# Kernel optimization log

Measured on AMD Instinct MI355X. Metric: run time of the kernel, lower is better.

The kernel has to match this reference:

```python
import jax, jax.numpy as jnp
import numpy as np

B = 128  # number of graphs/molecules in batch


def setup_inputs() -> dict:
    key = jax.random.key(0)
    ks = jax.random.split(key, 6)
    T, C, D = 131072, 512, 512  # total nodes, feature_dim, out_dim
    hidden_states = jax.random.normal(ks[0], (T, C), dtype=jnp.float32)
    data_batch = jnp.sort(jax.random.randint(ks[1], (T,), 0, B, dtype=jnp.int32))
    lim1 = 1.0 / np.sqrt(C)
    lim2 = 1.0 / np.sqrt(D)
    return {
        "hidden_states": hidden_states,
        "data_batch": data_batch,
        "max_nodes": 1280,
        "ln_gamma": jnp.ones((C,), jnp.float32),
        "ln_beta": jnp.zeros((C,), jnp.float32),
        "W1": jax.random.uniform(ks[2], (D, C), jnp.float32, -lim1, lim1),
        "b1": jax.random.uniform(ks[3], (D,), jnp.float32, -lim1, lim1),
        "W2": jax.random.uniform(ks[4], (D, D), jnp.float32, -lim2, lim2),
        "b2": jax.random.uniform(ks[5], (D,), jnp.float32, -lim2, lim2),
    }


def reference(hidden_states, data_batch, max_nodes, ln_gamma, ln_beta, W1, b1, W2, b2):
    T, C = hidden_states.shape
    # ragged -> dense scatter: position of each node within its batch group
    counts = jnp.bincount(data_batch, length=B)               # [B]
    offsets = jnp.cumsum(counts) - counts                      # exclusive cumsum [B]
    pos = jnp.arange(T, dtype=jnp.int32) - offsets[data_batch]  # [T]
    result = jnp.zeros((B, max_nodes, C), hidden_states.dtype).at[data_batch, pos].set(hidden_states)
    # mask: a padded row is all-zero
    mask = jnp.any(result != 0, axis=-1)[..., None].astype(result.dtype)  # [B, N, 1]
    # LayerNorm (eps=1e-5, torch default)
    mu = jnp.mean(result, axis=-1, keepdims=True)
    var = jnp.mean((result - mu) ** 2, axis=-1, keepdims=True)
    logits = (result - mu) * jax.lax.rsqrt(var + 1e-5) * ln_gamma + ln_beta
    cap_embes = logits @ W1.T + b1                              # [B, N, D]
    features_in = cap_embes @ W2.T + b2                         # [B, N, D]
    features_in = jnp.where(mask == 0, -10000.0, features_in)
    attn = jax.nn.softmax(features_in, axis=1)                  # softmax over nodes
    attn = jnp.where(mask == 0, 0.0, attn)
    return jnp.sum(attn * cap_embes, axis=1)                    # [B, D]
```

## Files before the change

### kernel.cpp

```cpp
#include <hip/hip_runtime.h>
#include <hip/hip_bf16.h>


typedef short short8 __attribute__((ext_vector_type(8)));
typedef short short4v __attribute__((ext_vector_type(4)));
typedef float f32x4 __attribute__((ext_vector_type(4)));

__device__ inline short f2bf(float f) {
    unsigned u = __float_as_uint(f);
    u += 0x7fffu + ((u >> 16) & 1u);
    return (short)(u >> 16);
}

__device__ inline size_t packed_off(int n, int k) {
    const int t = n >> 4, l16 = n & 15;
    const int k0 = k >> 5, quad = (k >> 3) & 3, j = k & 7;
    return ((size_t)((t * 16 + k0) * 64 + quad * 16 + l16)) * 8 + j;
}

#define PREP_GRID 229

__global__ __launch_bounds__(512)
void esa_prep_all(const float* __restrict__ W1, const float* __restrict__ W2,
                  const float* __restrict__ b1, const float* __restrict__ b2,
                  const int* __restrict__ db, int T, int B,
                  short* __restrict__ W1p, short* __restrict__ W12p,
                  float* __restrict__ b12, int4* __restrict__ entries, int maxent,
                  float* __restrict__ numden) {
    __shared__ int off[513];
    __shared__ int nch[512];
    __shared__ int scan[513];
    const int bid = blockIdx.x;
    const int tid = threadIdx.x;

    if (bid < 64) {
        const int ti = bid >> 3, tj = bid & 7;
        const int wave = tid >> 6;
        const int lane = tid & 63;
        const int quad = lane >> 4;
        const int l16 = lane & 15;
        const int mhalf = wave >> 2;
        const int kq = wave & 3;
        const int kcol = tj * 64 + kq * 16 + l16;

        f32x4 acc[2];
        acc[0] = (f32x4)0.0f; acc[1] = (f32x4)0.0f;
        for (int j0 = 0; j0 < 512; j0 += 32) {
            short8 bfr;
#pragma unroll
            for (int jj = 0; jj < 8; ++jj)
                bfr[jj] = f2bf(W1[(size_t)(j0 + quad * 8 + jj) * 512 + kcol]);
#pragma unroll
            for (int mt = 0; mt < 2; ++mt) {
                const float* ar = W2 + (size_t)(ti * 64 + (mhalf * 2 + mt) * 16 + l16) * 512 +
                                  j0 + quad * 8;
                const float4 a0 = *(const float4*)ar;
                const float4 a1 = *(const float4*)(ar + 4);
                short8 afr = {f2bf(a0.x), f2bf(a0.y), f2bf(a0.z), f2bf(a0.w),
                              f2bf(a1.x), f2bf(a1.y), f2bf(a1.z), f2bf(a1.w)};
                acc[mt] = __builtin_amdgcn_mfma_f32_16x16x32_bf16(afr, bfr,
                                                                  acc[mt], 0, 0, 0);
            }
        }
#pragma unroll
        for (int mt = 0; mt < 2; ++mt)
#pragma unroll
            for (int r = 0; r < 4; ++r) {
                const int n = ti * 64 + (mhalf * 2 + mt) * 16 + quad * 4 + r;
                W12p[packed_off(n, kcol)] = f2bf(acc[mt][r]);
            }
    } else if (bid < 192) {
        const int gid = (bid - 64) * 512 + tid;
        const int i4 = gid * 4;
        const int n = i4 >> 9, k = i4 & 511;
        const float4 a = *(const float4*)(W1 + i4);
        short4v sa = {f2bf(a.x), f2bf(a.y), f2bf(a.z), f2bf(a.w)};
        *(short4v*)(W1p + packed_off(n, k)) = sa;
    } else if (bid < 196) {
        const int row = (bid - 192) * 128 + (tid >> 2);
        const int part = tid & 3;
        const float* wr = W2 + (size_t)row * 512;
        float acc = 0.0f;
#pragma unroll 4
        for (int i = 0; i < 32; ++i) {
            const float4 w = *(const float4*)(wr + (i * 4 + part) * 4);
            const float4 bb = *(const float4*)(b1 + (i * 4 + part) * 4);
            acc += w.x * bb.x + w.y * bb.y + w.z * bb.z + w.w * bb.w;
        }
        acc += __shfl_xor(acc, 1);
        acc += __shfl_xor(acc, 2);
        if (part == 0) b12[row] = acc + b2[row];
    } else if (bid == 196) {
        for (int t = tid; t <= B; t += 512) {
            if (t == B) {
                off[t] = T;
            } else {
                int lo = 0, hi = T;
                while (lo < hi) {
                    int mid = (lo + hi) >> 1;
                    if (db[mid] < t) lo = mid + 1; else hi = mid;
                }
                off[t] = lo;
            }
        }
        __syncthreads();
        for (int t = tid; t < B; t += 512)
            nch[t] = (off[t + 1] - off[t] + 63) >> 6;
        __syncthreads();
        if (tid == 0) {
            int s = 0;
            for (int i = 0; i < B; ++i) { scan[i] = s; s += nch[i]; }
            scan[B] = s;
        }
        __syncthreads();
        for (int t = tid; t < B; t += 512) {
            int cnt = off[t + 1] - off[t];
            for (int j = 0; j < nch[t]; ++j) {
                int v = cnt - j * 64;
                if (v > 64) v = 64;
                entries[scan[t] + j] = make_int4(t, off[t] + j * 64, v, 0);
            }
        }
        int total = scan[B];
        for (int i = total + tid; i < maxent; i += 512)
            entries[i] = make_int4(0, 0, 0, 0);
    } else {
        const int idx = (bid - 197) * 512 + tid;
        float4 z = {0.0f, 0.0f, 0.0f, 0.0f};
        *(float4*)(numden + (size_t)idx * 8) = z;
        *(float4*)(numden + (size_t)idx * 8 + 4) = z;
    }
}

__global__ __launch_bounds__(512, 4)
void esa_fused(const float* __restrict__ x, const float* __restrict__ gamma,
               const float* __restrict__ beta, const short* __restrict__ W1p,
               const short* __restrict__ W12p, const float* __restrict__ b1,
               const float* __restrict__ b12, const int4* __restrict__ entries,
               float* __restrict__ num, float* __restrict__ den) {
    __shared__ short ylds[64 * 512];
    const int4 e = entries[blockIdx.x];
    const int bat = e.x, start = e.y, valid = e.z;
    if (valid <= 0) return;

    const int tid = threadIdx.x;
    const int wave = tid >> 6;
    const int lane = tid & 63;
    const int quad = lane >> 4;
    const int l16 = lane & 15;

    const float4 g0 = *(const float4*)(gamma + lane * 8);
    const float4 g1 = *(const float4*)(gamma + lane * 8 + 4);
    const float4 be0 = *(const float4*)(beta + lane * 8);
    const float4 be1 = *(const float4*)(beta + lane * 8 + 4);

#pragma unroll
    for (int g = 0; g < 2; ++g) {
        float4 ra[4], rb[4];
        float s[4], ss[4];
#pragma unroll
        for (int r = 0; r < 4; ++r) {
            const int m = wave * 8 + g * 4 + r;
            const int mc = m < valid ? m : valid - 1;
            const float* xr = x + (size_t)(start + mc) * 512 + lane * 8;
            ra[r] = *(const float4*)xr;
            rb[r] = *(const float4*)(xr + 4);
        }
#pragma unroll
        for (int r = 0; r < 4; ++r) {
            s[r] = ra[r].x + ra[r].y + ra[r].z + ra[r].w +
                   rb[r].x + rb[r].y + rb[r].z + rb[r].w;
            ss[r] = ra[r].x * ra[r].x + ra[r].y * ra[r].y + ra[r].z * ra[r].z +
                    ra[r].w * ra[r].w + rb[r].x * rb[r].x + rb[r].y * rb[r].y +
                    rb[r].z * rb[r].z + rb[r].w * rb[r].w;
        }
#pragma unroll
        for (int o = 1; o <= 32; o <<= 1) {
#pragma unroll
            for (int r = 0; r < 4; ++r) {
                s[r] += __shfl_xor(s[r], o);
                ss[r] += __shfl_xor(ss[r], o);
            }
        }
#pragma unroll
        for (int r = 0; r < 4; ++r) {
            const int m = wave * 8 + g * 4 + r;
            const float mu = s[r] * (1.0f / 512.0f);
            const float var = ss[r] * (1.0f / 512.0f) - mu * mu;
            const float rstd = rsqrtf(var + 1e-5f);
            short8 outv;
            outv[0] = f2bf((ra[r].x - mu) * rstd * g0.x + be0.x);
            outv[1] = f2bf((ra[r].y - mu) * rstd * g0.y + be0.y);
            outv[2] = f2bf((ra[r].z - mu) * rstd * g0.z + be0.z);
            outv[3] = f2bf((ra[r].w - mu) * rstd * g0.w + be0.w);
            outv[4] = f2bf((rb[r].x - mu) * rstd * g1.x + be1.x);
            outv[5] = f2bf((rb[r].y - mu) * rstd * g1.y + be1.y);
            outv[6] = f2bf((rb[r].z - mu) * rstd * g1.z + be1.z);
            outv[7] = f2bf((rb[r].w - mu) * rstd * g1.w + be1.w);
            *(short8*)&ylds[m * 512 + ((lane ^ (m & 7)) * 8)] = outv;
        }
    }
    __syncthreads();

    const int xr7 = l16 & 7;
    const short* abase = ylds + l16 * 512;

    for (int grp = 0; grp < 2; ++grp) {
        const int n0 = wave * 64 + grp * 32;
        const int ntile0 = n0 >> 4;
        f32x4 acc_c[2][4], acc_f[2][4];
#pragma unroll
        for (int nt = 0; nt < 2; ++nt)
#pragma unroll
            for (int mt = 0; mt < 4; ++mt) {
                acc_c[nt][mt] = (f32x4)0.0f;
                acc_f[nt][mt] = (f32x4)0.0f;
            }
        const short* w1t0 = W1p + (size_t)ntile0 * 8192 + lane * 8;
        const short* w1t1 = w1t0 + 8192;
        const short* w2t0 = W12p + (size_t)ntile0 * 8192 + lane * 8;
        const short* w2t1 = w2t0 + 8192;

#pragma unroll 2
        for (int k0 = 0; k0 < 16; ++k0) {
            const int blk = ((k0 << 2) | quad) ^ xr7;
            const short* ap = abase + blk * 8;
            short8 afr[4];
#pragma unroll
            for (int mt = 0; mt < 4; ++mt)
                afr[mt] = *(const short8*)(ap + mt * 16 * 512);
            const short8 b10 = *(const short8*)(w1t0 + k0 * 512);
            const short8 b11 = *(const short8*)(w1t1 + k0 * 512);
            const short8 b20 = *(const short8*)(w2t0 + k0 * 512);
            const short8 b21 = *(const short8*)(w2t1 + k0 * 512);
#pragma unroll
            for (int mt = 0; mt < 4; ++mt) {
                acc_c[0][mt] = __builtin_amdgcn_mfma_f32_16x16x32_bf16(
                    afr[mt], b10, acc_c[0][mt], 0, 0, 0);
                acc_c[1][mt] = __builtin_amdgcn_mfma_f32_16x16x32_bf16(
                    afr[mt], b11, acc_c[1][mt], 0, 0, 0);
                acc_f[0][mt] = __builtin_amdgcn_mfma_f32_16x16x32_bf16(
                    afr[mt], b20, acc_f[0][mt], 0, 0, 0);
                acc_f[1][mt] = __builtin_amdgcn_mfma_f32_16x16x32_bf16(
                    afr[mt], b21, acc_f[1][mt], 0, 0, 0);
            }
        }
#pragma unroll
        for (int nt = 0; nt < 2; ++nt) {
            const int n = n0 + nt * 16 + l16;
            const float bb1 = b1[n];
            const float bb2 = b12[n];
            float se = 0.0f, sec = 0.0f;
#pragma unroll
            for (int mt = 0; mt < 4; ++mt) {
#pragma unroll
                for (int r2 = 0; r2 < 4; ++r2) {
                    const int m = mt * 16 + quad * 4 + r2;
                    const float cap = acc_c[nt][mt][r2] + bb1;
                    const float ft = acc_f[nt][mt][r2] + bb2;
                    if (m < valid) {
                        const float ev = __expf(ft);
                        se += ev;
                        sec += ev * cap;
                    }
                }
            }
            se += __shfl_xor(se, 16);
            se += __shfl_xor(se, 32);
            sec += __shfl_xor(sec, 16);
            sec += __shfl_xor(sec, 32);
            if (quad == 0) atomicAdd(&den[(size_t)bat * 512 + n], se);
            else if (quad == 1) atomicAdd(&num[(size_t)bat * 512 + n], sec);
        }
    }
}

__global__ __launch_bounds__(256)
void esa_finalize(const float* __restrict__ num, const float* __restrict__ den,
                  float* __restrict__ out, int n) {
    const int i = blockIdx.x * 256 + threadIdx.x;
    if (i < n) {
        const float d = den[i];
        out[i] = d > 0.0f ? num[i] / d : 0.0f;
    }
}

extern "C" void kernel_launch(void* const* d_in, const int* in_sizes, int n_in,
                              void* d_out, int out_size, void* d_ws, size_t ws_size,
                              hipStream_t stream) {
    const float* x = (const float*)d_in[0];
    const int* db = (const int*)d_in[1];
    const float* gamma = (const float*)d_in[3];
    const float* beta = (const float*)d_in[4];
    const float* W1 = (const float*)d_in[5];
    const float* b1 = (const float*)d_in[6];
    const float* W2 = (const float*)d_in[7];
    const float* b2 = (const float*)d_in[8];
    float* out = (float*)d_out;

    const int C = in_sizes[3];
    const int D = in_sizes[6];
    const int T = in_sizes[0] / C;
    const int B = out_size / D;
    const int maxent = B + (T + 63) / 64;

    char* ws = (char*)d_ws;
    short* W1p = (short*)(ws);
    short* W12p = (short*)(ws + 524288);
    float* b12 = (float*)(ws + 1048576);
    int4* entries = (int4*)(ws + 1050624);
    size_t numoff = (1050624 + (size_t)maxent * 16 + 255) & ~(size_t)255;
    float* num = (float*)(ws + numoff);
    float* den = (float*)(ws + numoff + (size_t)B * D * 4);

    esa_prep_all<<<PREP_GRID, 512, 0, stream>>>(W1, W2, b1, b2, db, T, B,
                                                W1p, W12p, b12, entries, maxent,
                                                num);
    esa_fused<<<maxent, 512, 0, stream>>>(x, gamma, beta, W1p, W12p, b1, b12,
                                          entries, num, den);
    esa_finalize<<<(B * D + 255) / 256, 256, 0, stream>>>(num, den, out, B * D);
}
```

Baseline: 470.6 us.

## Make fused kernel persistent with atomic work queue and prefetch next chunk

```diff
diff --git a/kernel.cpp b/kernel.cpp
--- a/kernel.cpp
+++ b/kernel.cpp
@@ -13,9 +13,9 @@
 }
 
 __device__ inline size_t packed_off(int n, int k) {
-    const int t = n >> 4, l16 = n & 15;
+    const int t = n >> 4, l16n = n & 15;
     const int k0 = k >> 5, quad = (k >> 3) & 3, j = k & 7;
-    return ((size_t)((t * 16 + k0) * 64 + quad * 16 + l16)) * 8 + j;
+    return ((size_t)((t * 16 + k0) * 64 + quad * 16 + l16n)) * 8 + j;
 }
 
 #define PREP_GRID 229
@@ -26,7 +26,7 @@
                   const int* __restrict__ db, int T, int B,
                   short* __restrict__ W1p, short* __restrict__ W12p,
                   float* __restrict__ b12, int4* __restrict__ entries, int maxent,
-                  float* __restrict__ numden) {
+                  float* __restrict__ numden, int* __restrict__ ctrl) {
     __shared__ int off[513];
     __shared__ int nch[512];
     __shared__ int scan[513];
@@ -111,6 +111,8 @@
             int s = 0;
             for (int i = 0; i < B; ++i) { scan[i] = s; s += nch[i]; }
             scan[B] = s;
+            ctrl[0] = 0;
+            ctrl[1] = s;
         }
         __syncthreads();
         for (int t = tid; t < B; t += 512) {
@@ -137,131 +139,182 @@
                const float* __restrict__ beta, const short* __restrict__ W1p,
                const short* __restrict__ W12p, const float* __restrict__ b1,
                const float* __restrict__ b12, const int4* __restrict__ entries,
-               float* __restrict__ num, float* __restrict__ den) {
+               int* __restrict__ ctrl, float* __restrict__ num,
+               float* __restrict__ den) {
     __shared__ short ylds[64 * 512];
-    const int4 e = entries[blockIdx.x];
-    const int bat = e.x, start = e.y, valid = e.z;
-    if (valid <= 0) return;
+    __shared__ int4 ebuf[2];
+    __shared__ int eidx[2];
 
     const int tid = threadIdx.x;
     const int wave = tid >> 6;
     const int lane = tid & 63;
     const int quad = lane >> 4;
     const int l16 = lane & 15;
-
-    const float4 g0 = *(const float4*)(gamma + lane * 8);
-    const float4 g1 = *(const float4*)(gamma + lane * 8 + 4);
-    const float4 be0 = *(const float4*)(beta + lane * 8);
-    const float4 be1 = *(const float4*)(beta + lane * 8 + 4);
-
-#pragma unroll
-    for (int g = 0; g < 2; ++g) {
-        float4 ra[4], rb[4];
-        float s[4], ss[4];
+    const int total = ctrl[1];
+
+    if (tid == 0) {
+        const int j = atomicAdd(ctrl, 1);
+        eidx[0] = j;
+        ebuf[0] = entries[j < total ? j : total - 1];
+    }
+    __syncthreads();
+    if (eidx[0] >= total) return;
+    int4 ec = ebuf[0];
+    int bat = ec.x, start = ec.y, valid = ec.z;
+
+    float4 ra0[4], rb0[4], ra1[4], rb1[4];
+#pragma unroll
+    for (int r = 0; r < 4; ++r) {
+        const int m = wave * 8 + r;
+        const int mc = m < valid ? m : valid - 1;
+        const float* xr = x + (size_t)(start + mc) * 512 + lane * 8;
+        ra0[r] = *(const float4*)xr;
+        rb0[r] = *(const float4*)(xr + 4);
+    }
+
+    const int xr7 = l16 & 7;
+    const short* abase = ylds + l16 * 512;
+    int p = 0;
+
+    for (;;) {
 #pragma unroll
         for (int r = 0; r < 4; ++r) {
-            const int m = wave * 8 + g * 4 + r;
+            const int m = wave * 8 + 4 + r;
             const int mc = m < valid ? m : valid - 1;
             const float* xr = x + (size_t)(start + mc) * 512 + lane * 8;
-            ra[r] = *(const float4*)xr;
-            rb[r] = *(const float4*)(xr + 4);
-        }
+            ra1[r] = *(const float4*)xr;
+            rb1[r] = *(const float4*)(xr + 4);
+        }
+        const float4 g0 = *(const float4*)(gamma + lane * 8);
+        const float4 g1 = *(const float4*)(gamma + lane * 8 + 4);
+        const float4 be0 = *(const float4*)(beta + lane * 8);
+        const float4 be1 = *(const float4*)(beta + lane * 8 + 4);
+
+        auto lnpack = [&](const float4* A, const float4* Bv, short8* ov) {
+            float s[4], ss[4];
+#pragma unroll
+            for (int r = 0; r < 4; ++r) {
+                s[r] = A[r].x + A[r].y + A[r].z + A[r].w +
+                       Bv[r].x + Bv[r].y + Bv[r].z + Bv[r].w;
+                ss[r] = A[r].x * A[r].x + A[r].y * A[r].y + A[r].z * A[r].z +
+                        A[r].w * A[r].w + Bv[r].x * Bv[r].x + Bv[r].y * Bv[r].y +
+                        Bv[r].z * Bv[r].z + Bv[r].w * Bv[r].w;
+            }
+#pragma unroll
+            for (int o = 1; o <= 32; o <<= 1) {
+#pragma unroll
+                for (int r = 0; r < 4; ++r) {
+                    s[r] += __shfl_xor(s[r], o);
+                    ss[r] += __shfl_xor(ss[r], o);
+                }
+            }
+#pragma unroll
+            for (int r = 0; r < 4; ++r) {
+                const float mu = s[r] * (1.0f / 512.0f);
+                const float var = ss[r] * (1.0f / 512.0f) - mu * mu;
+                const float rstd = rsqrtf(var + 1e-5f);
+                short8 o8;
+                o8[0] = f2bf((A[r].x - mu) * rstd * g0.x + be0.x);
+                o8[1] = f2bf((A[r].y - mu) * rstd * g0.y + be0.y);
+                o8[2] = f2bf((A[r].z - mu) * rstd * g0.z + be0.z);
+                o8[3] = f2bf((A[r].w - mu) * rstd * g0.w + be0.w);
+                o8[4] = f2bf((Bv[r].x - mu) * rstd * g1.x + be1.x);
+                o8[5] = f2bf((Bv[r].y - mu) * rstd * g1.y + be1.y);
+                o8[6] = f2bf((Bv[r].z - mu) * rstd * g1.z + be1.z);
+                o8[7] = f2bf((Bv[r].w - mu) * rstd * g1.w + be1.w);
+                ov[r] = o8;
+            }
+        };
+
+        short8 ov0[4];
+        lnpack(ra0, rb0, ov0);
+
+        if (tid == 0) {
+            const int j = atomicAdd(ctrl, 1);
+            eidx[p ^ 1] = j;
+            ebuf[p ^ 1] = entries[j < total ? j : total - 1];
+        }
+        __syncthreads();
 #pragma unroll
         for (int r = 0; r < 4; ++r) {
-            s[r] = ra[r].x + ra[r].y + ra[r].z + ra[r].w +
-                   rb[r].x + rb[r].y + rb[r].z + rb[r].w;
-            ss[r] = ra[r].x * ra[r].x + ra[r].y * ra[r].y + ra[r].z * ra[r].z +
-                    ra[r].w * ra[r].w + rb[r].x * rb[r].x + rb[r].y * rb[r].y +
-                    rb[r].z * rb[r].z + rb[r].w * rb[r].w;
-        }
-#pragma unroll
-        for (int o = 1; o <= 32; o <<= 1) {
+            const int m = wave * 8 + r;
+            *(short8*)&ylds[m * 512 + ((lane ^ (m & 7)) * 8)] = ov0[r];
+        }
+        const int jn = eidx[p ^ 1];
+        const int4 en = ebuf[p ^ 1];
+        const bool have2 = (jn < total);
+        if (have2) {
 #pragma unroll
             for (int r = 0; r < 4; ++r) {
-                s[r] += __shfl_xor(s[r], o);
-                ss[r] += __shfl_xor(ss[r], o);
-            }
-        }
+                const int m = wave * 8 + r;
+                const int mc = m < en.z ? m : en.z - 1;
+                const float* xr = x + (size_t)(en.y + mc) * 512 + lane * 8;
+                ra0[r] = *(const float4*)xr;
+                rb0[r] = *(const float4*)(xr + 4);
+            }
+        }
+        short8 ov1[4];
+        lnpack(ra1, rb1, ov1);
 #pragma unroll
         for (int r = 0; r < 4; ++r) {
-            const int m = wave * 8 + g * 4 + r;
-            const float mu = s[r] * (1.0f / 512.0f);
-            const float var = ss[r] * (1.0f / 512.0f) - mu * mu;
-            const float rstd = rsqrtf(var + 1e-5f);
-            short8 outv;
-            outv[0] = f2bf((ra[r].x - mu) * rstd * g0.x + be0.x);
-            outv[1] = f2bf((ra[r].y - mu) * rstd * g0.y + be0.y);
-            outv[2] = f2bf((ra[r].z - mu) * rstd * g0.z + be0.z);
-            outv[3] = f2bf((ra[r].w - mu) * rstd * g0.w + be0.w);
-            outv[4] = f2bf((rb[r].x - mu) * rstd * g1.x + be1.x);
-            outv[5] = f2bf((rb[r].y - mu) * rstd * g1.y + be1.y);
-            outv[6] = f2bf((rb[r].z - mu) * rstd * g1.z + be1.z);
-            outv[7] = f2bf((rb[r].w - mu) * rstd * g1.w + be1.w);
-            *(short8*)&ylds[m * 512 + ((lane ^ (m & 7)) * 8)] = outv;
-        }
-    }
-    __syncthreads();
-
-    const int xr7 = l16 & 7;
-    const short* abase = ylds + l16 * 512;
-
-    for (int grp = 0; grp < 2; ++grp) {
-        const int n0 = wave * 64 + grp * 32;
-        const int ntile0 = n0 >> 4;
-        f32x4 acc_c[2][4], acc_f[2][4];
-#pragma unroll
-        for (int nt = 0; nt < 2; ++nt)
+            const int m = wave * 8 + 4 + r;
+            *(short8*)&ylds[m * 512 + ((lane ^ (m & 7)) * 8)] = ov1[r];
+        }
+        __syncthreads();
+
+#pragma unroll 1
+        for (int grp = 0; grp < 4; ++grp) {
+            const int ntile = wave * 4 + grp;
+            const short* w1 = W1p + (size_t)ntile * 8192 + lane * 8;
+            const short* w2 = W12p + (size_t)ntile * 8192 + lane * 8;
+            f32x4 acc_c[4], acc_f[4];
 #pragma unroll
             for (int mt = 0; mt < 4; ++mt) {
-                acc_c[nt][mt] = (f32x4)0.0f;
-                acc_f[nt][mt] = (f32x4)0.0f;
-            }
-        const short* w1t0 = W1p + (size_t)ntile0 * 8192 + lane * 8;
-        const short* w1t1 = w1t0 + 8192;
-        const short* w2t0 = W12p + (size_t)ntile0 * 8192 + lane * 8;
-        const short* w2t1 = w2t0 + 8192;
-
+                acc_c[mt] = (f32x4)0.0f;
+                acc_f[mt] = (f32x4)0.0f;
+            }
 #pragma unroll 2
-        for (int k0 = 0; k0 < 16; ++k0) {
-            const int blk = ((k0 << 2) | quad) ^ xr7;
-            const short* ap = abase + blk * 8;
-            short8 afr[4];
-#pragma unroll
-            for (int mt = 0; mt < 4; ++mt)
-                afr[mt] = *(const short8*)(ap + mt * 16 * 512);
-            const short8 b10 = *(const short8*)(w1t0 + k0 * 512);
-            const short8 b11 = *(const short8*)(w1t1 + k0 * 512);
-            const short8 b20 = *(const short8*)(w2t0 + k0 * 512);
-            const short8 b21 = *(const short8*)(w2t1 + k0 * 512);
-#pragma unroll
-            for (int mt = 0; mt < 4; ++mt) {
-                acc_c[0][mt] = __builtin_amdgcn_mfma_f32_16x16x32_bf16(
-                    afr[mt], b10, acc_c[0][mt], 0, 0, 0);
-                acc_c[1][mt] = __builtin_amdgcn_mfma_f32_16x16x32_bf16(
-                    afr[mt], b11, acc_c[1][mt], 0, 0, 0);
-                acc_f[0][mt] = __builtin_amdgcn_mfma_f32_16x16x32_bf16(
-                    afr[mt], b20, acc_f[0][mt], 0, 0, 0);
-                acc_f[1][mt] = __builtin_amdgcn_mfma_f32_16x16x32_bf16(
-                    afr[mt], b21, acc_f[1][mt], 0, 0, 0);
-            }
-        }
-#pragma unroll
-        for (int nt = 0; nt < 2; ++nt) {
-            const int n = n0 + nt * 16 + l16;
+            for (int k0 = 0; k0 < 16; ++k0) {
+                const int blk = ((k0 << 2) | quad) ^ xr7;
+                const short* ap = abase + blk * 8;
+                const short8 bc = *(const short8*)(w1 + k0 * 512);
+                const short8 bf = *(const short8*)(w2 + k0 * 512);
+                short8 afr[4];
+#pragma unroll
+                for (int mt = 0; mt < 4; ++mt)
+                    afr[mt] = *(const short8*)(ap + mt * 16 * 512);
+#pragma unroll
+                for (int mt = 0; mt < 4; ++mt) {
+                    acc_c[mt] = __builtin_amdgcn_mfma_f32_16x16x32_bf16(
+                        afr[mt], bc, acc_c[mt], 0, 0, 0);
+                    acc_f[mt] = __builtin_amdgcn_mfma_f32_16x16x32_bf16(
+                        afr[mt], bf, acc_f[mt], 0, 0, 0);
+                }
+            }
+            const int n = wave * 64 + grp * 16 + l16;
             const float bb1 = b1[n];
             const float bb2 = b12[n];
             float se = 0.0f, sec = 0.0f;
 #pragma unroll
             for (int mt = 0; mt < 4; ++mt) {
-#pragma unroll
-                for (int r2 = 0; r2 < 4; ++r2) {
-                    const int m = mt * 16 + quad * 4 + r2;
-                    const float cap = acc_c[nt][mt][r2] + bb1;
-                    const float ft = acc_f[nt][mt][r2] + bb2;
-                    if (m < valid) {
-                        const float ev = __expf(ft);
+                if ((mt + 1) * 16 <= valid) {
+#pragma unroll
+                    for (int r2 = 0; r2 < 4; ++r2) {
+                        const float cap = acc_c[mt][r2] + bb1;
+                        const float ev = __expf(acc_f[mt][r2] + bb2);
                         se += ev;
                         sec += ev * cap;
+                    }
+                } else if (mt * 16 < valid) {
+#pragma unroll
+                    for (int r2 = 0; r2 < 4; ++r2) {
+                        const int m = mt * 16 + quad * 4 + r2;
+                        if (m < valid) {
+                            const float cap = acc_c[mt][r2] + bb1;
+                            const float ev = __expf(acc_f[mt][r2] + bb2);
+                            se += ev;
+                            sec += ev * cap;
+                        }
                     }
                 }
             }
@@ -272,6 +325,10 @@
             if (quad == 0) atomicAdd(&den[(size_t)bat * 512 + n], se);
             else if (quad == 1) atomicAdd(&num[(size_t)bat * 512 + n], sec);
         }
+
+        bat = en.x; start = en.y; valid = en.z;
+        p ^= 1;
+        if (!have2) break;
     }
 }
 
@@ -309,14 +366,15 @@
     short* W12p = (short*)(ws + 524288);
     float* b12 = (float*)(ws + 1048576);
     int4* entries = (int4*)(ws + 1050624);
-    size_t numoff = (1050624 + (size_t)maxent * 16 + 255) & ~(size_t)255;
+    int* ctrl = (int*)(ws + 1050624 + (size_t)maxent * 16);
+    size_t numoff = (1050624 + (size_t)maxent * 16 + 8 + 255) & ~(size_t)255;
     float* num = (float*)(ws + numoff);
     float* den = (float*)(ws + numoff + (size_t)B * D * 4);
 
     esa_prep_all<<<PREP_GRID, 512, 0, stream>>>(W1, W2, b1, b2, db, T, B,
                                                 W1p, W12p, b12, entries, maxent,
-                                                num);
-    esa_fused<<<maxent, 512, 0, stream>>>(x, gamma, beta, W1p, W12p, b1, b12,
-                                          entries, num, den);
+                                                num, ctrl);
+    esa_fused<<<512, 512, 0, stream>>>(x, gamma, beta, W1p, W12p, b1, b12,
+                                       entries, ctrl, num, den);
     esa_finalize<<<(B * D + 255) / 256, 256, 0, stream>>>(num, den, out, B * D);
 }
```

Result: slower. 528.8 us (+12.4%).

## Switch fused kernel to 32x32x16 MFMA with persistent grid-stride blocks

Applied to the files above, without the earlier changes.

```diff
diff --git a/kernel.cpp b/kernel.cpp
--- a/kernel.cpp
+++ b/kernel.cpp
@@ -5,6 +5,7 @@
 typedef short short8 __attribute__((ext_vector_type(8)));
 typedef short short4v __attribute__((ext_vector_type(4)));
 typedef float f32x4 __attribute__((ext_vector_type(4)));
+typedef float f32x16 __attribute__((ext_vector_type(16)));
 
 __device__ inline short f2bf(float f) {
     unsigned u = __float_as_uint(f);
@@ -12,10 +13,10 @@
     return (short)(u >> 16);
 }
 
-__device__ inline size_t packed_off(int n, int k) {
-    const int t = n >> 4, l16 = n & 15;
-    const int k0 = k >> 5, quad = (k >> 3) & 3, j = k & 7;
-    return ((size_t)((t * 16 + k0) * 64 + quad * 16 + l16)) * 8 + j;
+__device__ inline size_t packed32_off(int n, int k) {
+    const int t = n >> 5, l31 = n & 31;
+    const int k0 = k >> 4, half = (k >> 3) & 1, j = k & 7;
+    return ((size_t)((t * 32 + k0) * 64 + half * 32 + l31)) * 8 + j;
 }
 
 #define PREP_GRID 229
@@ -67,7 +68,7 @@
 #pragma unroll
             for (int r = 0; r < 4; ++r) {
                 const int n = ti * 64 + (mhalf * 2 + mt) * 16 + quad * 4 + r;
-                W12p[packed_off(n, kcol)] = f2bf(acc[mt][r]);
+                W12p[packed32_off(n, kcol)] = f2bf(acc[mt][r]);
             }
     } else if (bid < 192) {
         const int gid = (bid - 64) * 512 + tid;
@@ -75,7 +76,7 @@
         const int n = i4 >> 9, k = i4 & 511;
         const float4 a = *(const float4*)(W1 + i4);
         short4v sa = {f2bf(a.x), f2bf(a.y), f2bf(a.z), f2bf(a.w)};
-        *(short4v*)(W1p + packed_off(n, k)) = sa;
+        *(short4v*)(W1p + packed32_off(n, k)) = sa;
     } else if (bid < 196) {
         const int row = (bid - 192) * 128 + (tid >> 2);
         const int part = tid & 3;
@@ -137,140 +138,138 @@
                const float* __restrict__ beta, const short* __restrict__ W1p,
                const short* __restrict__ W12p, const float* __restrict__ b1,
                const float* __restrict__ b12, const int4* __restrict__ entries,
-               float* __restrict__ num, float* __restrict__ den) {
+               int nent, float* __restrict__ num, float* __restrict__ den) {
     __shared__ short ylds[64 * 512];
-    const int4 e = entries[blockIdx.x];
-    const int bat = e.x, start = e.y, valid = e.z;
-    if (valid <= 0) return;
-
     const int tid = threadIdx.x;
     const int wave = tid >> 6;
     const int lane = tid & 63;
-    const int quad = lane >> 4;
-    const int l16 = lane & 15;
-
-    const float4 g0 = *(const float4*)(gamma + lane * 8);
-    const float4 g1 = *(const float4*)(gamma + lane * 8 + 4);
-    const float4 be0 = *(const float4*)(beta + lane * 8);
-    const float4 be1 = *(const float4*)(beta + lane * 8 + 4);
-
-#pragma unroll
-    for (int g = 0; g < 2; ++g) {
-        float4 ra[4], rb[4];
-        float s[4], ss[4];
-#pragma unroll
-        for (int r = 0; r < 4; ++r) {
-            const int m = wave * 8 + g * 4 + r;
-            const int mc = m < valid ? m : valid - 1;
-            const float* xr = x + (size_t)(start + mc) * 512 + lane * 8;
-            ra[r] = *(const float4*)xr;
-            rb[r] = *(const float4*)(xr + 4);
-        }
-#pragma unroll
-        for (int r = 0; r < 4; ++r) {
-            s[r] = ra[r].x + ra[r].y + ra[r].z + ra[r].w +
-                   rb[r].x + rb[r].y + rb[r].z + rb[r].w;
-            ss[r] = ra[r].x * ra[r].x + ra[r].y * ra[r].y + ra[r].z * ra[r].z +
-                    ra[r].w * ra[r].w + rb[r].x * rb[r].x + rb[r].y * rb[r].y +
-                    rb[r].z * rb[r].z + rb[r].w * rb[r].w;
-        }
-#pragma unroll
-        for (int o = 1; o <= 32; o <<= 1) {
+    const int l31 = lane & 31;
+    const int hi = lane >> 5;
+    const int xr = l31 & 15;
+    const short* abase = ylds + (size_t)l31 * 512;
+
+    for (int ent = blockIdx.x; ent < nent; ent += gridDim.x) {
+        const int4 e = entries[ent];
+        const int bat = e.x, start = e.y, valid = e.z;
+        if (valid <= 0) continue;
+
+        const float4 g0 = *(const float4*)(gamma + lane * 8);
+        const float4 g1 = *(const float4*)(gamma + lane * 8 + 4);
+        const float4 be0 = *(const float4*)(beta + lane * 8);
+        const float4 be1 = *(const float4*)(beta + lane * 8 + 4);
+
+#pragma unroll
+        for (int g = 0; g < 2; ++g) {
+            float4 ra[4], rb[4];
+            float s[4], ss[4];
 #pragma unroll
             for (int r = 0; r < 4; ++r) {
-                s[r] += __shfl_xor(s[r], o);
-                ss[r] += __shfl_xor(ss[r], o);
-            }
-        }
-#pragma unroll
-        for (int r = 0; r < 4; ++r) {
-            const int m = wave * 8 + g * 4 + r;
-            const float mu = s[r] * (1.0f / 512.0f);
-            const float var = ss[r] * (1.0f / 512.0f) - mu * mu;
-            const float rstd = rsqrtf(var + 1e-5f);
-            short8 outv;
-            outv[0] = f2bf((ra[r].x - mu) * rstd * g0.x + be0.x);
-            outv[1] = f2bf((ra[r].y - mu) * rstd * g0.y + be0.y);
-            outv[2] = f2bf((ra[r].z - mu) * rstd * g0.z + be0.z);
-            outv[3] = f2bf((ra[r].w - mu) * rstd * g0.w + be0.w);
-            outv[4] = f2bf((rb[r].x - mu) * rstd * g1.x + be1.x);
-            outv[5] = f2bf((rb[r].y - mu) * rstd * g1.y + be1.y);
-            outv[6] = f2bf((rb[r].z - mu) * rstd * g1.z + be1.z);
-            outv[7] = f2bf((rb[r].w - mu) * rstd * g1.w + be1.w);
-            *(short8*)&ylds[m * 512 + ((lane ^ (m & 7)) * 8)] = outv;
-        }
-    }
-    __syncthreads();
-
-    const int xr7 = l16 & 7;
-    const short* abase = ylds + l16 * 512;
-
-    for (int grp = 0; grp < 2; ++grp) {
-        const int n0 = wave * 64 + grp * 32;
-        const int ntile0 = n0 >> 4;
-        f32x4 acc_c[2][4], acc_f[2][4];
-#pragma unroll
-        for (int nt = 0; nt < 2; ++nt)
-#pragma unroll
-            for (int mt = 0; mt < 4; ++mt) {
-                acc_c[nt][mt] = (f32x4)0.0f;
-                acc_f[nt][mt] = (f32x4)0.0f;
-            }
-        const short* w1t0 = W1p + (size_t)ntile0 * 8192 + lane * 8;
-        const short* w1t1 = w1t0 + 8192;
-        const short* w2t0 = W12p + (size_t)ntile0 * 8192 + lane * 8;
-        const short* w2t1 = w2t0 + 8192;
-
-#pragma unroll 2
-        for (int k0 = 0; k0 < 16; ++k0) {
-            const int blk = ((k0 << 2) | quad) ^ xr7;
-            const short* ap = abase + blk * 8;
-            short8 afr[4];
-#pragma unroll
-            for (int mt = 0; mt < 4; ++mt)
-                afr[mt] = *(const short8*)(ap + mt * 16 * 512);
-            const short8 b10 = *(const short8*)(w1t0 + k0 * 512);
-            const short8 b11 = *(const short8*)(w1t1 + k0 * 512);
-            const short8 b20 = *(const short8*)(w2t0 + k0 * 512);
-            const short8 b21 = *(const short8*)(w2t1 + k0 * 512);
-#pragma unroll
-            for (int mt = 0; mt < 4; ++mt) {
-                acc_c[0][mt] = __builtin_amdgcn_mfma_f32_16x16x32_bf16(
-                    afr[mt], b10, acc_c[0][mt], 0, 0, 0);
-                acc_c[1][mt] = __builtin_amdgcn_mfma_f32_16x16x32_bf16(
-                    afr[mt], b11, acc_c[1][mt], 0, 0, 0);
-                acc_f[0][mt] = __builtin_amdgcn_mfma_f32_16x16x32_bf16(
-                    afr[mt], b20, acc_f[0][mt], 0, 0, 0);
-                acc_f[1][mt] = __builtin_amdgcn_mfma_f32_16x16x32_bf16(
-                    afr[mt], b21, acc_f[1][mt], 0, 0, 0);
-            }
-        }
-#pragma unroll
-        for (int nt = 0; nt < 2; ++nt) {
-            const int n = n0 + nt * 16 + l16;
+                const int m = wave * 8 + g * 4 + r;
+                const int mc = m < valid ? m : valid - 1;
+                const float* xr_ = x + (size_t)(start + mc) * 512 + lane * 8;
+                ra[r] = *(const float4*)xr_;
+                rb[r] = *(const float4*)(xr_ + 4);
+            }
+#pragma unroll
+            for (int r = 0; r < 4; ++r) {
+                s[r] = ra[r].x + ra[r].y + ra[r].z + ra[r].w +
+                       rb[r].x + rb[r].y + rb[r].z + rb[r].w;
+                ss[r] = ra[r].x * ra[r].x + ra[r].y * ra[r].y + ra[r].z * ra[r].z +
+                        ra[r].w * ra[r].w + rb[r].x * rb[r].x + rb[r].y * rb[r].y +
+                        rb[r].z * rb[r].z + rb[r].w * rb[r].w;
+            }
+#pragma unroll
+            for (int o = 1; o <= 32; o <<= 1) {
+#pragma unroll
+                for (int r = 0; r < 4; ++r) {
+                    s[r] += __shfl_xor(s[r], o);
+                    ss[r] += __shfl_xor(ss[r], o);
+                }
+            }
+            if (g == 0) __syncthreads();
+#pragma unroll
+            for (int r = 0; r < 4; ++r) {
+                const int m = wave * 8 + g * 4 + r;
+                const float mu = s[r] * (1.0f / 512.0f);
+                const float var = ss[r] * (1.0f / 512.0f) - mu * mu;
+                const float rstd = rsqrtf(var + 1e-5f);
+                short8 outv;
+                outv[0] = f2bf((ra[r].x - mu) * rstd * g0.x + be0.x);
+                outv[1] = f2bf((ra[r].y - mu) * rstd * g0.y + be0.y);
+                outv[2] = f2bf((ra[r].z - mu) * rstd * g0.z + be0.z);
+                outv[3] = f2bf((ra[r].w - mu) * rstd * g0.w + be0.w);
+                outv[4] = f2bf((rb[r].x - mu) * rstd * g1.x + be1.x);
+                outv[5] = f2bf((rb[r].y - mu) * rstd * g1.y + be1.y);
+                outv[6] = f2bf((rb[r].z - mu) * rstd * g1.z + be1.z);
+                outv[7] = f2bf((rb[r].w - mu) * rstd * g1.w + be1.w);
+                *(short8*)&ylds[m * 512 + ((lane ^ (m & 15)) * 8)] = outv;
+            }
+        }
+        __syncthreads();
+
+        const bool full = (valid >= 64);
+
+        for (int grp = 0; grp < 2; ++grp) {
+            const int nt32 = wave * 2 + grp;
+            const short* w1 = W1p + (size_t)nt32 * 16384 + lane * 8;
+            const short* w2 = W12p + (size_t)nt32 * 16384 + lane * 8;
+            f32x16 acc_c[2], acc_f[2];
+#pragma unroll
+            for (int mt = 0; mt < 2; ++mt) {
+                acc_c[mt] = (f32x16)0.0f;
+                acc_f[mt] = (f32x16)0.0f;
+            }
+#pragma unroll 4
+            for (int ks = 0; ks < 32; ++ks) {
+                const int blk = ((ks << 1) | hi) ^ xr;
+                const short* ap = abase + blk * 8;
+                const short8 a0 = *(const short8*)(ap);
+                const short8 a1 = *(const short8*)(ap + 32 * 512);
+                const short8 bc = *(const short8*)(w1 + ks * 512);
+                const short8 bf = *(const short8*)(w2 + ks * 512);
+                acc_c[0] = __builtin_amdgcn_mfma_f32_32x32x16_bf16(
+                    a0, bc, acc_c[0], 0, 0, 0);
+                acc_c[1] = __builtin_amdgcn_mfma_f32_32x32x16_bf16(
+                    a1, bc, acc_c[1], 0, 0, 0);
+                acc_f[0] = __builtin_amdgcn_mfma_f32_32x32x16_bf16(
+                    a0, bf, acc_f[0], 0, 0, 0);
+                acc_f[1] = __builtin_amdgcn_mfma_f32_32x32x16_bf16(
+                    a1, bf, acc_f[1], 0, 0, 0);
+            }
+            const int n = wave * 64 + grp * 32 + l31;
             const float bb1 = b1[n];
             const float bb2 = b12[n];
             float se = 0.0f, sec = 0.0f;
-#pragma unroll
-            for (int mt = 0; mt < 4; ++mt) {
-#pragma unroll
-                for (int r2 = 0; r2 < 4; ++r2) {
-                    const int m = mt * 16 + quad * 4 + r2;
-                    const float cap = acc_c[nt][mt][r2] + bb1;
-                    const float ft = acc_f[nt][mt][r2] + bb2;
-                    if (m < valid) {
-                        const float ev = __expf(ft);
+            if (full) {
+#pragma unroll
+                for (int mt = 0; mt < 2; ++mt) {
+#pragma unroll
+                    for (int r = 0; r < 16; ++r) {
+                        const float cap = acc_c[mt][r] + bb1;
+                        const float ev = __expf(acc_f[mt][r] + bb2);
                         se += ev;
                         sec += ev * cap;
                     }
                 }
-            }
-            se += __shfl_xor(se, 16);
+            } else {
+#pragma unroll
+                for (int mt = 0; mt < 2; ++mt) {
+#pragma unroll
+                    for (int r = 0; r < 16; ++r) {
+                        const int m = mt * 32 + (r & 3) + 8 * (r >> 2) + 4 * hi;
+                        if (m < valid) {
+                            const float cap = acc_c[mt][r] + bb1;
+                            const float ev = __expf(acc_f[mt][r] + bb2);
+                            se += ev;
+                            sec += ev * cap;
+                        }
+                    }
+                }
+            }
             se += __shfl_xor(se, 32);
-            sec += __shfl_xor(sec, 16);
             sec += __shfl_xor(sec, 32);
-            if (quad == 0) atomicAdd(&den[(size_t)bat * 512 + n], se);
-            else if (quad == 1) atomicAdd(&num[(size_t)bat * 512 + n], sec);
+            if (hi == 0) atomicAdd(&den[(size_t)bat * 512 + n], se);
+            else atomicAdd(&num[(size_t)bat * 512 + n], sec);
         }
     }
 }
@@ -316,7 +315,7 @@
     esa_prep_all<<<PREP_GRID, 512, 0, stream>>>(W1, W2, b1, b2, db, T, B,
                                                 W1p, W12p, b12, entries, maxent,
                                                 num);
-    esa_fused<<<maxent, 512, 0, stream>>>(x, gamma, beta, W1p, W12p, b1, b12,
-                                          entries, num, den);
+    esa_fused<<<512, 512, 0, stream>>>(x, gamma, beta, W1p, W12p, b1, b12,
+                                       entries, maxent, num, den);
     esa_finalize<<<(B * D + 255) / 256, 256, 0, stream>>>(num, den, out, B * D);
 }
```

Measured after the change: 505.9 us. +7.5%, slower.

## Split LayerNorm staging into halves and overlap second half with first GEMM

Applied to the files above, without the earlier changes.

```diff
diff --git a/kernel.cpp b/kernel.cpp
--- a/kernel.cpp
+++ b/kernel.cpp
@@ -13,9 +13,9 @@
 }
 
 __device__ inline size_t packed_off(int n, int k) {
-    const int t = n >> 4, l16 = n & 15;
+    const int t = n >> 4, l16n = n & 15;
     const int k0 = k >> 5, quad = (k >> 3) & 3, j = k & 7;
-    return ((size_t)((t * 16 + k0) * 64 + quad * 16 + l16)) * 8 + j;
+    return ((size_t)((t * 16 + k0) * 64 + quad * 16 + l16n)) * 8 + j;
 }
 
 #define PREP_GRID 229
@@ -154,25 +154,15 @@
     const float4 be0 = *(const float4*)(beta + lane * 8);
     const float4 be1 = *(const float4*)(beta + lane * 8 + 4);
 
-#pragma unroll
-    for (int g = 0; g < 2; ++g) {
-        float4 ra[4], rb[4];
+    auto lnstore = [&](const float4* A, const float4* Bv, int mbase) {
         float s[4], ss[4];
 #pragma unroll
         for (int r = 0; r < 4; ++r) {
-            const int m = wave * 8 + g * 4 + r;
-            const int mc = m < valid ? m : valid - 1;
-            const float* xr = x + (size_t)(start + mc) * 512 + lane * 8;
-            ra[r] = *(const float4*)xr;
-            rb[r] = *(const float4*)(xr + 4);
-        }
-#pragma unroll
-        for (int r = 0; r < 4; ++r) {
-            s[r] = ra[r].x + ra[r].y + ra[r].z + ra[r].w +
-                   rb[r].x + rb[r].y + rb[r].z + rb[r].w;
-            ss[r] = ra[r].x * ra[r].x + ra[r].y * ra[r].y + ra[r].z * ra[r].z +
-                    ra[r].w * ra[r].w + rb[r].x * rb[r].x + rb[r].y * rb[r].y +
-                    rb[r].z * rb[r].z + rb[r].w * rb[r].w;
+            s[r] = A[r].x + A[r].y + A[r].z + A[r].w +
+                   Bv[r].x + Bv[r].y + Bv[r].z + Bv[r].w;
+            ss[r] = A[r].x * A[r].x + A[r].y * A[r].y + A[r].z * A[r].z +
+                    A[r].w * A[r].w + Bv[r].x * Bv[r].x + Bv[r].y * Bv[r].y +
+                    Bv[r].z * Bv[r].z + Bv[r].w * Bv[r].w;
         }
 #pragma unroll
         for (int o = 1; o <= 32; o <<= 1) {
@@ -184,43 +174,166 @@
         }
 #pragma unroll
         for (int r = 0; r < 4; ++r) {
-            const int m = wave * 8 + g * 4 + r;
+            const int m = mbase + wave * 4 + r;
             const float mu = s[r] * (1.0f / 512.0f);
             const float var = ss[r] * (1.0f / 512.0f) - mu * mu;
             const float rstd = rsqrtf(var + 1e-5f);
             short8 outv;
-            outv[0] = f2bf((ra[r].x - mu) * rstd * g0.x + be0.x);
-            outv[1] = f2bf((ra[r].y - mu) * rstd * g0.y + be0.y);
-            outv[2] = f2bf((ra[r].z - mu) * rstd * g0.z + be0.z);
-            outv[3] = f2bf((ra[r].w - mu) * rstd * g0.w + be0.w);
-            outv[4] = f2bf((rb[r].x - mu) * rstd * g1.x + be1.x);
-            outv[5] = f2bf((rb[r].y - mu) * rstd * g1.y + be1.y);
-            outv[6] = f2bf((rb[r].z - mu) * rstd * g1.z + be1.z);
-            outv[7] = f2bf((rb[r].w - mu) * rstd * g1.w + be1.w);
+            outv[0] = f2bf((A[r].x - mu) * rstd * g0.x + be0.x);
+            outv[1] = f2bf((A[r].y - mu) * rstd * g0.y + be0.y);
+            outv[2] = f2bf((A[r].z - mu) * rstd * g0.z + be0.z);
+            outv[3] = f2bf((A[r].w - mu) * rstd * g0.w + be0.w);
+            outv[4] = f2bf((Bv[r].x - mu) * rstd * g1.x + be1.x);
+            outv[5] = f2bf((Bv[r].y - mu) * rstd * g1.y + be1.y);
+            outv[6] = f2bf((Bv[r].z - mu) * rstd * g1.z + be1.z);
+            outv[7] = f2bf((Bv[r].w - mu) * rstd * g1.w + be1.w);
             *(short8*)&ylds[m * 512 + ((lane ^ (m & 7)) * 8)] = outv;
         }
+    };
+
+    float4 ra[4], rb[4], ra1[4], rb1[4];
+#pragma unroll
+    for (int r = 0; r < 4; ++r) {
+        const int m = wave * 4 + r;
+        const int mc = m < valid ? m : valid - 1;
+        const float* p = x + (size_t)(start + mc) * 512 + lane * 8;
+        ra[r] = *(const float4*)p;
+        rb[r] = *(const float4*)(p + 4);
+    }
+    lnstore(ra, rb, 0);
+
+#pragma unroll
+    for (int r = 0; r < 4; ++r) {
+        const int m = 32 + wave * 4 + r;
+        const int mc = m < valid ? m : valid - 1;
+        const float* p = x + (size_t)(start + mc) * 512 + lane * 8;
+        ra1[r] = *(const float4*)p;
+        rb1[r] = *(const float4*)(p + 4);
     }
     __syncthreads();
 
     const int xr7 = l16 & 7;
     const short* abase = ylds + l16 * 512;
-
-    for (int grp = 0; grp < 2; ++grp) {
-        const int n0 = wave * 64 + grp * 32;
-        const int ntile0 = n0 >> 4;
-        f32x4 acc_c[2][4], acc_f[2][4];
-#pragma unroll
-        for (int nt = 0; nt < 2; ++nt)
-#pragma unroll
-            for (int mt = 0; mt < 4; ++mt) {
-                acc_c[nt][mt] = (f32x4)0.0f;
-                acc_f[nt][mt] = (f32x4)0.0f;
-            }
+    const bool full = (valid >= 64);
+
+    auto epi = [&](const f32x4 (&ac)[2][4], const f32x4 (&af)[2][4], int n0) {
+#pragma unroll
+        for (int nt = 0; nt < 2; ++nt) {
+            const int n = n0 + nt * 16 + l16;
+            const float bb1 = b1[n];
+            const float bb2 = b12[n];
+            float se = 0.0f, sec = 0.0f;
+            if (full) {
+#pragma unroll
+                for (int mt = 0; mt < 4; ++mt) {
+#pragma unroll
+                    for (int r2 = 0; r2 < 4; ++r2) {
+                        const float cap = ac[nt][mt][r2] + bb1;
+                        const float ev = __expf(af[nt][mt][r2] + bb2);
+                        se += ev;
+                        sec += ev * cap;
+                    }
+                }
+            } else {
+#pragma unroll
+                for (int mt = 0; mt < 4; ++mt) {
+#pragma unroll
+                    for (int r2 = 0; r2 < 4; ++r2) {
+                        const int m = mt * 16 + quad * 4 + r2;
+                        if (m < valid) {
+                            const float cap = ac[nt][mt][r2] + bb1;
+                            const float ev = __expf(af[nt][mt][r2] + bb2);
+                            se += ev;
+                            sec += ev * cap;
+                        }
+                    }
+                }
+            }
+            se += __shfl_xor(se, 16);
+            se += __shfl_xor(se, 32);
+            sec += __shfl_xor(sec, 16);
+            sec += __shfl_xor(sec, 32);
+            if (quad == 0) atomicAdd(&den[(size_t)bat * 512 + n], se);
+            else if (quad == 1) atomicAdd(&num[(size_t)bat * 512 + n], sec);
+        }
+    };
+
+    {
+        const int ntile0 = wave * 4;
         const short* w1t0 = W1p + (size_t)ntile0 * 8192 + lane * 8;
         const short* w1t1 = w1t0 + 8192;
         const short* w2t0 = W12p + (size_t)ntile0 * 8192 + lane * 8;
         const short* w2t1 = w2t0 + 8192;
 
+        f32x4 acc_c[2][4], acc_f[2][4];
+#pragma unroll
+        for (int nt = 0; nt < 2; ++nt)
+#pragma unroll
+            for (int mt = 0; mt < 4; ++mt) {
+                acc_c[nt][mt] = (f32x4)0.0f;
+                acc_f[nt][mt] = (f32x4)0.0f;
+            }
+
+#pragma unroll 2
+        for (int k0 = 0; k0 < 16; ++k0) {
+            const int blk = ((k0 << 2) | quad) ^ xr7;
+            const short* ap = abase + blk * 8;
+            const short8 af0 = *(const short8*)(ap);
+            const short8 af1 = *(const short8*)(ap + 16 * 512);
+            const short8 b10 = *(const short8*)(w1t0 + k0 * 512);
+            const short8 b11 = *(const short8*)(w1t1 + k0 * 512);
+            const short8 b20 = *(const short8*)(w2t0 + k0 * 512);
+            const short8 b21 = *(const short8*)(w2t1 + k0 * 512);
+            acc_c[0][0] = __builtin_amdgcn_mfma_f32_16x16x32_bf16(af0, b10, acc_c[0][0], 0, 0, 0);
+            acc_c[0][1] = __builtin_amdgcn_mfma_f32_16x16x32_bf16(af1, b10, acc_c[0][1], 0, 0, 0);
+            acc_c[1][0] = __builtin_amdgcn_mfma_f32_16x16x32_bf16(af0, b11, acc_c[1][0], 0, 0, 0);
+            acc_c[1][1] = __builtin_amdgcn_mfma_f32_16x16x32_bf16(af1, b11, acc_c[1][1], 0, 0, 0);
+            acc_f[0][0] = __builtin_amdgcn_mfma_f32_16x16x32_bf16(af0, b20, acc_f[0][0], 0, 0, 0);
+            acc_f[0][1] = __builtin_amdgcn_mfma_f32_16x16x32_bf16(af1, b20, acc_f[0][1], 0, 0, 0);
+            acc_f[1][0] = __builtin_amdgcn_mfma_f32_16x16x32_bf16(af0, b21, acc_f[1][0], 0, 0, 0);
+            acc_f[1][1] = __builtin_amdgcn_mfma_f32_16x16x32_bf16(af1, b21, acc_f[1][1], 0, 0, 0);
+        }
+
+        lnstore(ra1, rb1, 32);
+        __syncthreads();
+
+#pragma unroll 2
+        for (int k0 = 0; k0 < 16; ++k0) {
+            const int blk = ((k0 << 2) | quad) ^ xr7;
+            const short* ap = abase + blk * 8;
+            const short8 af2 = *(const short8*)(ap + 32 * 512);
+            const short8 af3 = *(const short8*)(ap + 48 * 512);
+            const short8 b10 = *(const short8*)(w1t0 + k0 * 512);
+            const short8 b11 = *(const short8*)(w1t1 + k0 * 512);
+            const short8 b20 = *(const short8*)(w2t0 + k0 * 512);
+            const short8 b21 = *(const short8*)(w2t1 + k0 * 512);
+            acc_c[0][2] = __builtin_amdgcn_mfma_f32_16x16x32_bf16(af2, b10, acc_c[0][2], 0, 0, 0);
+            acc_c[0][3] = __builtin_amdgcn_mfma_f32_16x16x32_bf16(af3, b10, acc_c[0][3], 0, 0, 0);
+            acc_c[1][2] = __builtin_amdgcn_mfma_f32_16x16x32_bf16(af2, b11, acc_c[1][2], 0, 0, 0);
+            acc_c[1][3] = __builtin_amdgcn_mfma_f32_16x16x32_bf16(af3, b11, acc_c[1][3], 0, 0, 0);
+            acc_f[0][2] = __builtin_amdgcn_mfma_f32_16x16x32_bf16(af2, b20, acc_f[0][2], 0, 0, 0);
+            acc_f[0][3] = __builtin_amdgcn_mfma_f32_16x16x32_bf16(af3, b20, acc_f[0][3], 0, 0, 0);
+            acc_f[1][2] = __builtin_amdgcn_mfma_f32_16x16x32_bf16(af2, b21, acc_f[1][2], 0, 0, 0);
+            acc_f[1][3] = __builtin_amdgcn_mfma_f32_16x16x32_bf16(af3, b21, acc_f[1][3], 0, 0, 0);
+        }
+        epi(acc_c, acc_f, wave * 64);
+    }
+
+    {
+        const int ntile0 = wave * 4 + 2;
+        const short* w1t0 = W1p + (size_t)ntile0 * 8192 + lane * 8;
+        const short* w1t1 = w1t0 + 8192;
+        const short* w2t0 = W12p + (size_t)ntile0 * 8192 + lane * 8;
+        const short* w2t1 = w2t0 + 8192;
+
+        f32x4 acc_c[2][4], acc_f[2][4];
+#pragma unroll
+        for (int nt = 0; nt < 2; ++nt)
+#pragma unroll
+            for (int mt = 0; mt < 4; ++mt) {
+                acc_c[nt][mt] = (f32x4)0.0f;
+                acc_f[nt][mt] = (f32x4)0.0f;
+            }
 #pragma unroll 2
         for (int k0 = 0; k0 < 16; ++k0) {
             const int blk = ((k0 << 2) | quad) ^ xr7;
@@ -245,33 +358,7 @@
                     afr[mt], b21, acc_f[1][mt], 0, 0, 0);
             }
         }
-#pragma unroll
-        for (int nt = 0; nt < 2; ++nt) {
-            const int n = n0 + nt * 16 + l16;
-            const float bb1 = b1[n];
-            const float bb2 = b12[n];
-            float se = 0.0f, sec = 0.0f;
-#pragma unroll
-            for (int mt = 0; mt < 4; ++mt) {
-#pragma unroll
-                for (int r2 = 0; r2 < 4; ++r2) {
-                    const int m = mt * 16 + quad * 4 + r2;
-                    const float cap = acc_c[nt][mt][r2] + bb1;
-                    const float ft = acc_f[nt][mt][r2] + bb2;
-                    if (m < valid) {
-                        const float ev = __expf(ft);
-                        se += ev;
-                        sec += ev * cap;
-                    }
-                }
-            }
-            se += __shfl_xor(se, 16);
-            se += __shfl_xor(se, 32);
-            sec += __shfl_xor(sec, 16);
-            sec += __shfl_xor(sec, 32);
-            if (quad == 0) atomicAdd(&den[(size_t)bat * 512 + n], se);
-            else if (quad == 1) atomicAdd(&num[(size_t)bat * 512 + n], sec);
-        }
+        epi(acc_c, acc_f, wave * 64 + 32);
     }
 }
 
```

Result: slower. 528.5 us (+12.3%).
